# Optimization experiments

Measured on AMD Instinct MI355X. Metric: run time of the kernel, lower is better.

The kernel has to match this reference:

```python
import jax, jax.numpy as jnp
import numpy as np

B, N, D, H, P = 8, 1025, 768, 12, 32  # n = P*P + 1 (CLS + patches)
HD = D // H
EPS = 1e-5


def setup_inputs() -> dict:
    key = jax.random.key(0)
    ks = jax.random.split(key, 6)
    return {
        "x": jax.random.normal(ks[0], (B, N, D), dtype=jnp.float32),
        "canny": jax.random.uniform(ks[1], (B, 1, P, P), dtype=jnp.float32),
        "noise": jax.random.uniform(ks[2], (B, P, P), dtype=jnp.float32),
        "ln_w": jnp.ones((D,), dtype=jnp.float32),
        "ln_b": jnp.zeros((D,), dtype=jnp.float32),
        "w_qkv": (jax.random.normal(ks[3], (D, 3 * D), dtype=jnp.float32) * 0.02),
        "w_out": (jax.random.normal(ks[4], (D, D), dtype=jnp.float32) * 0.02),
        "b_out": jnp.zeros((D,), dtype=jnp.float32),
    }


def reference(x, canny, noise, ln_w, ln_b, w_qkv, w_out, b_out):
    b, n, d = x.shape
    # LayerNorm
    mu = jnp.mean(x, axis=-1, keepdims=True)
    var = jnp.mean(jnp.square(x - mu), axis=-1, keepdims=True)
    x_norm = (x - mu) * jax.lax.rsqrt(var + EPS) * ln_w + ln_b
    # QKV projection (no bias), split into heads: [b, n, 3, h, hd]
    qkv = (x_norm @ w_qkv).reshape(b, n, 3, H, HD)
    q = jnp.transpose(qkv[:, :, 0], (0, 2, 1, 3))  # [b, h, n, hd]
    k = jnp.transpose(qkv[:, :, 1], (0, 2, 1, 3))
    v = jnp.transpose(qkv[:, :, 2], (0, 2, 1, 3))
    # NOTE: source uses scale = dim ** -0.5 (full dim, not head_dim)
    dots = jnp.einsum('bhid,bhjd->bhij', q, k) * (d ** -0.5)
    # CLS-row prior injection: softmax over patch keys of CLS query row
    attn_row = jax.nn.softmax(dots[:, :, 0, 1:], axis=-1)  # [b, h, n-1]
    canny_flat = canny.reshape(b, -1) + 1.0                # [b, n-1]
    canny_flat = canny_flat / jnp.sum(canny_flat, axis=-1, keepdims=True)
    noise_flat = noise.reshape(b, -1)                      # [b, n-1]
    noise_flat = noise_flat / jnp.sum(noise_flat, axis=-1, keepdims=True)
    attn_row = attn_row + canny_flat[:, None, :] + noise_flat[:, None, :]
    dots = dots.at[:, :, 0, 1:].set(attn_row)
    # Second (full) softmax; dropout is identity in eval mode
    attn = jax.nn.softmax(dots, axis=-1)
    out = jnp.einsum('bhij,bhjd->bhid', attn, v)           # [b, h, n, hd]
    out = jnp.transpose(out, (0, 2, 1, 3)).reshape(b, n, d)
    return out @ w_out + b_out
```

## Files before the change

### kernel.cpp

```cpp
#include <hip/hip_runtime.h>

#define B_ 8
#define N_ 1025
#define D_ 768
#define H_ 12
#define NP_ 1024
#define ROWS_ (B_*N_)
#define ROWS_PAD_ 8320
#define QKVC_ 2304
#define SCALE_ 0.03608439182435161f
#define EPS_ 1e-5f

typedef float f32x4 __attribute__((ext_vector_type(4)));
typedef short s16x8 __attribute__((ext_vector_type(8)));

#define GLD16(g, l) __builtin_amdgcn_global_load_lds( \
    (const __attribute__((address_space(1))) unsigned int*)(g), \
    (__attribute__((address_space(3))) unsigned int*)(l), 16, 0, 0)

__device__ __forceinline__ float blo(unsigned int u){
  union { unsigned int i; float f; } v; v.i = u << 16; return v.f;
}
__device__ __forceinline__ float bhi(unsigned int u){
  union { unsigned int i; float f; } v; v.i = u & 0xffff0000u; return v.f;
}
__device__ __forceinline__ float bf2f(unsigned short u){
  union { unsigned int i; float f; } v; v.i = ((unsigned int)u) << 16; return v.f;
}
__device__ __forceinline__ unsigned short f2bf(float f){
  union { unsigned int i; float f; } v; v.f = f;
  unsigned int b = v.i;
  b = b + 0x7fffu + ((b >> 16) & 1u);
  return (unsigned short)(b >> 16);
}
__device__ __forceinline__ unsigned int pkbf2(float a, float b){
  union { float f; unsigned int i; } ua, ub;
  ua.f = a; ub.f = b;
  return __builtin_amdgcn_perm(ub.i + 0x8000u, ua.i + 0x8000u, 0x07060302u);
}

__global__ __launch_bounds__(256) void prep_fused(
    const float* __restrict__ w1, unsigned short* __restrict__ d1,
    const float* __restrict__ w2, unsigned short* __restrict__ d2,
    const float* __restrict__ x, const float* __restrict__ lw,
    const float* __restrict__ lb, unsigned short* __restrict__ xn) {
  int id = blockIdx.x;
  int t = threadIdx.x;
  if (id < 2304) {
    __shared__ unsigned short tile[32][33];
    int bx = id % 96;
    int kb = (id / 96) * 32;
    const float* src; unsigned short* dst; int N, nb;
    if (bx < 72) { src = w1; dst = d1; N = QKVC_; nb = bx * 32; }
    else         { src = w2; dst = d2; N = D_;    nb = (bx - 72) * 32; }
    int tx = t & 31, ty = t >> 5;
    #pragma unroll
    for (int i = 0; i < 4; i++) {
      int r = ty + i * 8;
      tile[r][tx] = f2bf(src[(size_t)(kb + r) * N + nb + tx]);
    }
    __syncthreads();
    #pragma unroll
    for (int i = 0; i < 4; i++) {
      int r = ty + i * 8;
      dst[(size_t)(nb + r) * D_ + kb + tx] = tile[tx][r];
    }
  } else {
    int row = id - 2304;
    __shared__ float r6[6];
    float4 v; float s = 0.f, q = 0.f;
    if (t < 192) {
      v = ((const float4*)(x + (size_t)row * D_))[t];
      s = v.x + v.y + v.z + v.w;
      q = v.x * v.x + v.y * v.y + v.z * v.z + v.w * v.w;
      #pragma unroll
      for (int off = 32; off > 0; off >>= 1) {
        s += __shfl_xor(s, off, 64);
        q += __shfl_xor(q, off, 64);
      }
      if ((t & 63) == 0) { r6[t >> 6] = s; r6[3 + (t >> 6)] = q; }
    }
    __syncthreads();
    if (t < 192) {
      s = r6[0] + r6[1] + r6[2];
      q = r6[3] + r6[4] + r6[5];
      float mean = s * (1.0f / 768.0f);
      float var = q * (1.0f / 768.0f) - mean * mean;
      var = var < 0.f ? 0.f : var;
      float rstd = rsqrtf(var + EPS_);
      float4 wv4 = ((const float4*)lw)[t];
      float4 bv4 = ((const float4*)lb)[t];
      float o0 = (v.x - mean) * rstd * wv4.x + bv4.x;
      float o1 = (v.y - mean) * rstd * wv4.y + bv4.y;
      float o2 = (v.z - mean) * rstd * wv4.z + bv4.z;
      float o3 = (v.w - mean) * rstd * wv4.w + bv4.w;
      uint2 pk = {pkbf2(o0, o1), pkbf2(o2, o3)};
      *(uint2*)(xn + (size_t)row * D_ + t * 4) = pk;
    }
  }
}

template <bool OF32>
__global__ __launch_bounds__(512) void gemm_bt(
    const unsigned short* __restrict__ A, const unsigned short* __restrict__ Bt,
    void* __restrict__ Cv, const float* __restrict__ bias,
    int Mvalid, int Nn, int Kk) {
  __shared__ short sh[32768];
  int t = threadIdx.x;
  int lane = t & 63, w = t >> 6;
  int m16 = lane & 15, quad = lane >> 4;

  int nwg = gridDim.x;
  int nbx = Nn >> 7;
  int id = blockIdx.x;
  int qq = nwg >> 3, rr = nwg & 7;
  int xcd = id & 7, off = id >> 3;
  int wg = (xcd < rr ? xcd * (qq + 1) : rr * (qq + 1) + (xcd - rr) * qq) + off;
  int bx = wg % nbx, by = wg / nbx;
  int bm = by * 128, bn = bx * 128;

  int wm = (w & 1) * 64, wn = (w >> 1) * 32;

  f32x4 acc[4][2];
  #pragma unroll
  for (int i = 0; i < 4; i++)
    #pragma unroll
    for (int j = 0; j < 2; j++) acc[i][j] = (f32x4){0.f, 0.f, 0.f, 0.f};

  const unsigned short* aP[2];
  const unsigned short* bP[2];
  #pragma unroll
  for (int c = 0; c < 2; c++) {
    int g = t + c * 512;
    int row = g >> 3, slot = g & 7;
    aP[c] = A  + (size_t)(bm + row) * Kk + ((slot ^ (row & 7)) * 8);
    bP[c] = Bt + (size_t)(bn + row) * Kk + ((slot ^ (row & 7)) * 8);
  }

  int KS = Kk >> 6;
  int cur = 0;
  #pragma unroll
  for (int c = 0; c < 2; c++) GLD16(aP[c], sh + (t + c * 512) * 8);
  #pragma unroll
  for (int c = 0; c < 2; c++) GLD16(bP[c], sh + 16384 + (t + c * 512) * 8);

  for (int kt = 0; kt < KS; kt++) {
    asm volatile("s_waitcnt vmcnt(0)" ::: "memory");
    __builtin_amdgcn_s_barrier();
    if (kt + 1 < KS) {
      int nb2 = (cur ^ 1) * 8192;
      int ko = (kt + 1) * 64;
      #pragma unroll
      for (int c = 0; c < 2; c++) GLD16(aP[c] + ko, sh + nb2 + (t + c * 512) * 8);
      #pragma unroll
      for (int c = 0; c < 2; c++) GLD16(bP[c] + ko, sh + 16384 + nb2 + (t + c * 512) * 8);
    }
    const short* sa = sh + cur * 8192;
    const short* sb = sh + 16384 + cur * 8192;
    #pragma unroll
    for (int ks = 0; ks < 2; ks++) {
      int so = ((ks * 4 + quad) ^ (m16 & 7)) * 8;
      s16x8 af[4], bfr[2];
      #pragma unroll
      for (int i = 0; i < 4; i++)
        af[i] = *(const s16x8*)(sa + (wm + i * 16 + m16) * 64 + so);
      #pragma unroll
      for (int j = 0; j < 2; j++)
        bfr[j] = *(const s16x8*)(sb + (wn + j * 16 + m16) * 64 + so);
      __builtin_amdgcn_s_setprio(1);
      #pragma unroll
      for (int i = 0; i < 4; i++)
        #pragma unroll
        for (int j = 0; j < 2; j++)
          acc[i][j] = __builtin_amdgcn_mfma_f32_16x16x32_bf16(af[i], bfr[j], acc[i][j], 0, 0, 0);
      __builtin_amdgcn_s_setprio(0);
    }
    cur ^= 1;
  }
  __syncthreads();

  if (!OF32) {
    unsigned short* C = (unsigned short*)Cv;
    #pragma unroll
    for (int j = 0; j < 2; j++) {
      int col = wn + j * 16 + m16;
      #pragma unroll
      for (int i = 0; i < 4; i++)
        #pragma unroll
        for (int r = 0; r < 4; r++)
          sh[(wm + i * 16 + quad * 4 + r) * 128 + col] = (short)f2bf(acc[i][j][r]);
    }
    __syncthreads();
    #pragma unroll
    for (int c = 0; c < 4; c++) {
      int idx = c * 512 + t;
      int row = idx >> 4, col = (idx & 15) * 8;
      if (bm + row < Mvalid)
        *(uint4*)(&C[(size_t)(bm + row) * Nn + bn + col]) = *(const uint4*)(&sh[row * 128 + col]);
    }
  } else {
    float* Cf = (float*)Cv;
    float* shf = (float*)sh;
    #pragma unroll
    for (int j = 0; j < 2; j++) {
      int col = wn + j * 16 + m16;
      float bv = bias ? bias[bn + col] : 0.f;
      #pragma unroll
      for (int i = 0; i < 4; i++)
        #pragma unroll
        for (int r = 0; r < 4; r++)
          shf[(wm + i * 16 + quad * 4 + r) * 128 + col] = acc[i][j][r] + bv;
    }
    __syncthreads();
    #pragma unroll
    for (int c = 0; c < 8; c++) {
      int idx = c * 512 + t;
      int row = idx >> 5, col = (idx & 31) * 4;
      if (bm + row < Mvalid)
        *(float4*)(&Cf[(size_t)(bm + row) * Nn + bn + col]) =
            *(const float4*)(&shf[row * 128 + col]);
    }
  }
}

__device__ __forceinline__ float block_sum(float v, float* red) {
  int t = threadIdx.x;
  red[t] = v;
  __syncthreads();
  for (int st = 128; st > 0; st >>= 1) {
    if (t < st) red[t] += red[t + st];
    __syncthreads();
  }
  float r = red[0];
  __syncthreads();
  return r;
}

__global__ __launch_bounds__(256) void attn_fused(
    const unsigned short* __restrict__ qkv, const float* __restrict__ canny,
    const float* __restrict__ noise, unsigned short* __restrict__ attn_out) {
  __shared__ __align__(16) char pool[37888];
  int id = blockIdx.x;
  int t = threadIdx.x;

  if (id < 768) {
    short* ps = (short*)pool;
    short* ks = (short*)(pool + 18432);
    unsigned int* vs = (unsigned int*)(pool + 27648);
    float* tailbuf = (float*)(pool + 36864);

    int tile = id / 96;
    int rem = id % 96;
    int h = rem >> 3;
    int b = rem & 7;
    int lane = t & 63, w = t >> 6;
    int m16 = lane & 15, quad = lane >> 4;

    int qbase = 1 + tile * 128;

    {
      int r = t >> 1, seg = (t & 1) * 32;
      const uint4* src = (const uint4*)(qkv + (size_t)(b * N_ + qbase + r) * QKVC_ + h * 64 + seg);
      uint4 u0 = src[0], u1 = src[1], u2 = src[2], u3 = src[3];
      *(uint4*)(&ps[r * 72 + seg])      = u0;
      *(uint4*)(&ps[r * 72 + seg + 8])  = u1;
      *(uint4*)(&ps[r * 72 + seg + 16]) = u2;
      *(uint4*)(&ps[r * 72 + seg + 24]) = u3;
    }
    s16x8 qb[2][2];
    #pragma unroll
    for (int nt = 0; nt < 2; nt++)
      #pragma unroll
      for (int ks_ = 0; ks_ < 2; ks_++) {
        qb[nt][ks_] = *(const s16x8*)(&ps[(w * 32 + nt * 16 + m16) * 72 + ks_ * 32 + quad * 8]);
        unsigned int* u = (unsigned int*)&qb[nt][ks_];
        #pragma unroll
        for (int i = 0; i < 4; i++)
          u[i] = pkbf2(blo(u[i]) * SCALE_, bhi(u[i]) * SCALE_);
      }
    s16x8 vone;
    #pragma unroll
    for (int i = 0; i < 8; i++) vone[i] = (short)0x3F80;

    f32x4 oacc[2][4], lacc[2];
    #pragma unroll
    for (int mt = 0; mt < 2; mt++) {
      lacc[mt] = (f32x4){0.f, 0.f, 0.f, 0.f};
      #pragma unroll
      for (int dt = 0; dt < 4; dt++) oacc[mt][dt] = (f32x4){0.f, 0.f, 0.f, 0.f};
    }

    int kkey = t >> 2, kseg = (t & 3) * 16;
    const unsigned short* kbase = qkv + (size_t)(b * N_) * QKVC_ + D_ + h * 64;
    int vp2 = t & 31, vseg = t >> 5;
    const unsigned short* vbase = qkv + (size_t)(b * N_) * QKVC_ + 2 * D_ + h * 64 + vseg * 8;
    uint4 kr0, kr1, vr0, vr1;
    {
      const uint4* ksrc = (const uint4*)(kbase + (size_t)kkey * QKVC_ + kseg);
      kr0 = ksrc[0]; kr1 = ksrc[1];
      vr0 = *(const uint4*)(vbase + (size_t)(2 * vp2) * QKVC_);
      vr1 = *(const uint4*)(vbase + (size_t)(2 * vp2 + 1) * QKVC_);
    }

    for (int jt = 0; jt < 16; jt++) {
      __syncthreads();
      *(uint4*)(&ks[kkey * 72 + kseg])     = kr0;
      *(uint4*)(&ks[kkey * 72 + kseg + 8]) = kr1;
      {
        const unsigned int* vaw = (const unsigned int*)&vr0;
        const unsigned int* vbw = (const unsigned int*)&vr1;
        #pragma unroll
        for (int i = 0; i < 4; i++) {
          vs[(vseg * 8 + 2 * i)     * 36 + vp2] = __builtin_amdgcn_perm(vbw[i], vaw[i], 0x05040100u);
          vs[(vseg * 8 + 2 * i + 1) * 36 + vp2] = __builtin_amdgcn_perm(vbw[i], vaw[i], 0x07060302u);
        }
      }
      __syncthreads();
      if (jt < 15) {
        int j0 = (jt + 1) * 64;
        const uint4* ksrc = (const uint4*)(kbase + (size_t)(j0 + kkey) * QKVC_ + kseg);
        kr0 = ksrc[0]; kr1 = ksrc[1];
        vr0 = *(const uint4*)(vbase + (size_t)(j0 + 2 * vp2) * QKVC_);
        vr1 = *(const uint4*)(vbase + (size_t)(j0 + 2 * vp2 + 1) * QKVC_);
      }
      f32x4 sacc[4][2];
      #pragma unroll
      for (int kt = 0; kt < 4; kt++) {
        s16x8 ka0 = *(const s16x8*)(&ks[(kt * 16 + m16) * 72 + quad * 8]);
        s16x8 ka1 = *(const s16x8*)(&ks[(kt * 16 + m16) * 72 + 32 + quad * 8]);
        #pragma unroll
        for (int nt = 0; nt < 2; nt++) {
          f32x4 s = (f32x4){0.f, 0.f, 0.f, 0.f};
          s = __builtin_amdgcn_mfma_f32_16x16x32_bf16(ka0, qb[nt][0], s, 0, 0, 0);
          s = __builtin_amdgcn_mfma_f32_16x16x32_bf16(ka1, qb[nt][1], s, 0, 0, 0);
          sacc[kt][nt] = s;
        }
      }
      #pragma unroll
      for (int kt = 0; kt < 4; kt++) {
        #pragma unroll
        for (int nt = 0; nt < 2; nt++) {
          f32x4 s = sacc[kt][nt];
          float p0 = __expf(s[0]);
          float p1 = __expf(s[1]);
          float p2 = __expf(s[2]);
          float p3 = __expf(s[3]);
          uint2 pk = {pkbf2(p0, p1), pkbf2(p2, p3)};
          *(uint2*)(&ps[(w * 32 + nt * 16 + m16) * 72 + kt * 16 + quad * 4]) = pk;
        }
      }
      __syncthreads();
      s16x8 pa[2][2];
      #pragma unroll
      for (int mt = 0; mt < 2; mt++)
        #pragma unroll
        for (int ks_ = 0; ks_ < 2; ks_++)
          pa[mt][ks_] = *(const s16x8*)(&ps[(w * 32 + mt * 16 + m16) * 72 + ks_ * 32 + quad * 8]);
      const short* vss = (const short*)vs;
      #pragma unroll
      for (int dt = 0; dt < 4; dt++) {
        s16x8 vb0 = *(const s16x8*)(&vss[(dt * 16 + m16) * 72 + quad * 8]);
        s16x8 vb1 = *(const s16x8*)(&vss[(dt * 16 + m16) * 72 + 32 + quad * 8]);
        #pragma unroll
        for (int mt = 0; mt < 2; mt++) {
          oacc[mt][dt] = __builtin_amdgcn_mfma_f32_16x16x32_bf16(pa[mt][0], vb0, oacc[mt][dt], 0, 0, 0);
          oacc[mt][dt] = __builtin_amdgcn_mfma_f32_16x16x32_bf16(pa[mt][1], vb1, oacc[mt][dt], 0, 0, 0);
        }
      }
      #pragma unroll
      for (int mt = 0; mt < 2; mt++) {
        lacc[mt] = __builtin_amdgcn_mfma_f32_16x16x32_bf16(pa[mt][0], vone, lacc[mt], 0, 0, 0);
        lacc[mt] = __builtin_amdgcn_mfma_f32_16x16x32_bf16(pa[mt][1], vone, lacc[mt], 0, 0, 0);
      }
    }
    if (t < 64)       tailbuf[t]             = bf2f(qkv[(size_t)(b * N_ + 1024) * QKVC_ + D_     + h * 64 + t]);
    else if (t < 128) tailbuf[64 + (t - 64)] = bf2f(qkv[(size_t)(b * N_ + 1024) * QKVC_ + 2 * D_ + h * 64 + (t - 64)]);
    __syncthreads();
    #pragma unroll
    for (int nt = 0; nt < 2; nt++) {
      float d = 0.f;
      #pragma unroll
      for (int jj = 0; jj < 8; jj++) {
        d += bf2f((unsigned short)qb[nt][0][jj]) * tailbuf[quad * 8 + jj];
        d += bf2f((unsigned short)qb[nt][1][jj]) * tailbuf[32 + quad * 8 + jj];
      }
      d += __shfl_xor(d, 16, 64);
      d += __shfl_xor(d, 32, 64);
      float p = __expf(d);
      if (quad == 0) tailbuf[128 + w * 32 + nt * 16 + m16] = p;
    }
    __syncthreads();
    #pragma unroll
    for (int mt = 0; mt < 2; mt++)
      #pragma unroll
      for (int r = 0; r < 4; r++) {
        float pr = tailbuf[128 + w * 32 + mt * 16 + quad * 4 + r];
        lacc[mt][r] += pr;
        #pragma unroll
        for (int dt = 0; dt < 4; dt++)
          oacc[mt][dt][r] += pr * tailbuf[64 + dt * 16 + m16];
      }
    #pragma unroll
    for (int mt = 0; mt < 2; mt++) {
      float rinv[4];
      #pragma unroll
      for (int r = 0; r < 4; r++) rinv[r] = 1.0f / lacc[mt][r];
      #pragma unroll
      for (int dt = 0; dt < 4; dt++) {
        #pragma unroll
        for (int r = 0; r < 4; r++) {
          int grow = b * N_ + qbase + w * 32 + mt * 16 + quad * 4 + r;
          attn_out[(size_t)grow * D_ + h * 64 + dt * 16 + m16] = f2bf(oacc[mt][dt][r] * rinv[r]);
        }
      }
    }
  } else {
    float* s     = (float*)pool;
    float* red   = (float*)(pool + 4608);
    float* q     = (float*)(pool + 5632);
    float* pvred = (float*)(pool + 5888);

    int bh = id - 768;
    int b = bh / H_, h = bh % H_;

    if (t < 64) q[t] = bf2f(qkv[(size_t)(b * N_) * QKVC_ + h * 64 + t]);
    __syncthreads();

    for (int j = t; j < N_; j += 256) {
      const unsigned short* krow = qkv + (size_t)(b * N_ + j) * QKVC_ + D_ + h * 64;
      float dot = 0.f;
      #pragma unroll
      for (int c = 0; c < 8; c++) {
        uint4 kk = *(const uint4*)(krow + c * 8);
        dot += q[c*8+0]*blo(kk.x) + q[c*8+1]*bhi(kk.x)
             + q[c*8+2]*blo(kk.y) + q[c*8+3]*bhi(kk.y)
             + q[c*8+4]*blo(kk.z) + q[c*8+5]*bhi(kk.z)
             + q[c*8+6]*blo(kk.w) + q[c*8+7]*bhi(kk.w);
      }
      s[j] = dot * SCALE_;
    }
    float cp = 0.f, npp = 0.f;
    for (int j = t; j < NP_; j += 256) {
      cp  += canny[b * NP_ + j] + 1.0f;
      npp += noise[b * NP_ + j];
    }
    float csum = block_sum(cp, red);
    float nsum = block_sum(npp, red);
    float e1 = 0.f;
    for (int j = t; j < N_; j += 256) if (j >= 1) e1 += __expf(s[j]);
    float sum1 = block_sum(e1, red);
    for (int j = t; j < N_; j += 256) {
      if (j >= 1) {
        s[j] = __expf(s[j]) / sum1
             + (canny[b * NP_ + j - 1] + 1.0f) / csum
             + noise[b * NP_ + j - 1] / nsum;
      }
    }
    __syncthreads();
    float e2 = 0.f;
    for (int j = t; j < N_; j += 256) { float e = __expf(s[j]); s[j] = e; e2 += e; }
    float sum2 = block_sum(e2, red);
    {
      int o = t & 7, g = t >> 3;
      float a[8] = {0.f, 0.f, 0.f, 0.f, 0.f, 0.f, 0.f, 0.f};
      for (int j = g; j < N_; j += 32) {
        float sv = s[j];
        uint4 vv = *(const uint4*)(qkv + (size_t)(b * N_ + j) * QKVC_ + 2 * D_ + h * 64 + o * 8);
        a[0] += sv * blo(vv.x); a[1] += sv * bhi(vv.x);
        a[2] += sv * blo(vv.y); a[3] += sv * bhi(vv.y);
        a[4] += sv * blo(vv.z); a[5] += sv * bhi(vv.z);
        a[6] += sv * blo(vv.w); a[7] += sv * bhi(vv.w);
      }
      #pragma unroll
      for (int i = 0; i < 8; i++) pvred[(o * 8 + i) * 33 + g] = a[i];
    }
    __syncthreads();
    if (t < 64) {
      float acc = 0.f;
      #pragma unroll
      for (int u = 0; u < 32; u++) acc += pvred[t * 33 + u];
      attn_out[(size_t)(b * N_) * D_ + h * 64 + t] = f2bf(acc / sum2);
    }
  }
}

extern "C" void kernel_launch(void* const* d_in, const int* in_sizes, int n_in,
                              void* d_out, int out_size, void* d_ws, size_t ws_size,
                              hipStream_t stream) {
  (void)in_sizes; (void)n_in; (void)out_size; (void)ws_size;
  const float* x     = (const float*)d_in[0];
  const float* canny = (const float*)d_in[1];
  const float* noise = (const float*)d_in[2];
  const float* lnw   = (const float*)d_in[3];
  const float* lnb   = (const float*)d_in[4];
  const float* wqkv  = (const float*)d_in[5];
  const float* wout  = (const float*)d_in[6];
  const float* bout  = (const float*)d_in[7];
  float* out = (float*)d_out;
  char* ws = (char*)d_ws;

  unsigned short* xn    = (unsigned short*)(ws);
  unsigned short* wqkvT = (unsigned short*)(ws + 12779520);
  unsigned short* woutT = (unsigned short*)(ws + 16318464);
  unsigned short* qkv   = (unsigned short*)(ws + 17498112);

  prep_fused<<<dim3(2304 + ROWS_), 256, 0, stream>>>(
      wqkv, wqkvT, wout, woutT, x, lnw, lnb, xn);
  gemm_bt<false><<<dim3((QKVC_ / 128) * (ROWS_PAD_ / 128)), 512, 0, stream>>>(
      xn, wqkvT, (void*)qkv, nullptr, ROWS_, QKVC_, D_);
  attn_fused<<<dim3(768 + B_ * H_), 256, 0, stream>>>(qkv, canny, noise, xn);
  gemm_bt<true><<<dim3((D_ / 128) * (ROWS_PAD_ / 128)), 512, 0, stream>>>(
      xn, woutT, (void*)out, bout, ROWS_, D_, D_);
}
```

Measured before the change: 198.2 us.

## Use 512-thread attention blocks with one 16-row query tile per wave

Doubles the attention kernel's block size from 256 to 512 threads, so each of 8 waves handles 16 query rows instead of 32. K/V tile loads, the CLS-row path and the reductions are re-partitioned across the extra threads, and the reduction scratch offsets grow to match. The aim is more waves in flight to hide latency and fewer registers per wave. In exchange each wave has less MFMA work per K/V tile, and syncs now span a larger block.

After: 210.8 us. 6.4% more time.

```diff
diff --git a/kernel.cpp b/kernel.cpp
--- a/kernel.cpp
+++ b/kernel.cpp
@@ -223,11 +223,11 @@
   }
 }
 
-__device__ __forceinline__ float block_sum(float v, float* red) {
+__device__ __forceinline__ float block_sum512(float v, float* red) {
   int t = threadIdx.x;
   red[t] = v;
   __syncthreads();
-  for (int st = 128; st > 0; st >>= 1) {
+  for (int st = 256; st > 0; st >>= 1) {
     if (t < st) red[t] += red[t + st];
     __syncthreads();
   }
@@ -236,7 +236,7 @@
   return r;
 }
 
-__global__ __launch_bounds__(256) void attn_fused(
+__global__ __launch_bounds__(512) void attn_fused(
     const unsigned short* __restrict__ qkv, const float* __restrict__ canny,
     const float* __restrict__ noise, unsigned short* __restrict__ attn_out) {
   __shared__ __align__(16) char pool[37888];
@@ -259,166 +259,138 @@
     int qbase = 1 + tile * 128;
 
     {
-      int r = t >> 1, seg = (t & 1) * 32;
+      int r = t >> 2, seg = (t & 3) * 16;
       const uint4* src = (const uint4*)(qkv + (size_t)(b * N_ + qbase + r) * QKVC_ + h * 64 + seg);
-      uint4 u0 = src[0], u1 = src[1], u2 = src[2], u3 = src[3];
-      *(uint4*)(&ps[r * 72 + seg])      = u0;
-      *(uint4*)(&ps[r * 72 + seg + 8])  = u1;
-      *(uint4*)(&ps[r * 72 + seg + 16]) = u2;
-      *(uint4*)(&ps[r * 72 + seg + 24]) = u3;
-    }
-    s16x8 qb[2][2];
-    #pragma unroll
-    for (int nt = 0; nt < 2; nt++)
-      #pragma unroll
-      for (int ks_ = 0; ks_ < 2; ks_++) {
-        qb[nt][ks_] = *(const s16x8*)(&ps[(w * 32 + nt * 16 + m16) * 72 + ks_ * 32 + quad * 8]);
-        unsigned int* u = (unsigned int*)&qb[nt][ks_];
-        #pragma unroll
-        for (int i = 0; i < 4; i++)
-          u[i] = pkbf2(blo(u[i]) * SCALE_, bhi(u[i]) * SCALE_);
-      }
+      uint4 u0 = src[0], u1 = src[1];
+      *(uint4*)(&ps[r * 72 + seg])     = u0;
+      *(uint4*)(&ps[r * 72 + seg + 8]) = u1;
+    }
+    s16x8 qb[2];
+    #pragma unroll
+    for (int ks_ = 0; ks_ < 2; ks_++) {
+      qb[ks_] = *(const s16x8*)(&ps[(w * 16 + m16) * 72 + ks_ * 32 + quad * 8]);
+      unsigned int* u = (unsigned int*)&qb[ks_];
+      #pragma unroll
+      for (int i = 0; i < 4; i++)
+        u[i] = pkbf2(blo(u[i]) * SCALE_, bhi(u[i]) * SCALE_);
+    }
     s16x8 vone;
     #pragma unroll
     for (int i = 0; i < 8; i++) vone[i] = (short)0x3F80;
 
-    f32x4 oacc[2][4], lacc[2];
-    #pragma unroll
-    for (int mt = 0; mt < 2; mt++) {
-      lacc[mt] = (f32x4){0.f, 0.f, 0.f, 0.f};
-      #pragma unroll
-      for (int dt = 0; dt < 4; dt++) oacc[mt][dt] = (f32x4){0.f, 0.f, 0.f, 0.f};
-    }
-
-    int kkey = t >> 2, kseg = (t & 3) * 16;
+    f32x4 oacc[4], lacc;
+    lacc = (f32x4){0.f, 0.f, 0.f, 0.f};
+    #pragma unroll
+    for (int dt = 0; dt < 4; dt++) oacc[dt] = (f32x4){0.f, 0.f, 0.f, 0.f};
+
+    int kkey = t >> 3, kseg = (t & 7) * 8;
     const unsigned short* kbase = qkv + (size_t)(b * N_) * QKVC_ + D_ + h * 64;
     int vp2 = t & 31, vseg = t >> 5;
-    const unsigned short* vbase = qkv + (size_t)(b * N_) * QKVC_ + 2 * D_ + h * 64 + vseg * 8;
-    uint4 kr0, kr1, vr0, vr1;
+    const unsigned short* vbase = qkv + (size_t)(b * N_) * QKVC_ + 2 * D_ + h * 64 + vseg * 4;
+    uint4 kr0; uint2 vr0, vr1;
     {
-      const uint4* ksrc = (const uint4*)(kbase + (size_t)kkey * QKVC_ + kseg);
-      kr0 = ksrc[0]; kr1 = ksrc[1];
-      vr0 = *(const uint4*)(vbase + (size_t)(2 * vp2) * QKVC_);
-      vr1 = *(const uint4*)(vbase + (size_t)(2 * vp2 + 1) * QKVC_);
+      kr0 = *(const uint4*)(kbase + (size_t)kkey * QKVC_ + kseg);
+      vr0 = *(const uint2*)(vbase + (size_t)(2 * vp2) * QKVC_);
+      vr1 = *(const uint2*)(vbase + (size_t)(2 * vp2 + 1) * QKVC_);
     }
 
     for (int jt = 0; jt < 16; jt++) {
       __syncthreads();
-      *(uint4*)(&ks[kkey * 72 + kseg])     = kr0;
-      *(uint4*)(&ks[kkey * 72 + kseg + 8]) = kr1;
+      *(uint4*)(&ks[kkey * 72 + kseg]) = kr0;
       {
         const unsigned int* vaw = (const unsigned int*)&vr0;
         const unsigned int* vbw = (const unsigned int*)&vr1;
         #pragma unroll
-        for (int i = 0; i < 4; i++) {
-          vs[(vseg * 8 + 2 * i)     * 36 + vp2] = __builtin_amdgcn_perm(vbw[i], vaw[i], 0x05040100u);
-          vs[(vseg * 8 + 2 * i + 1) * 36 + vp2] = __builtin_amdgcn_perm(vbw[i], vaw[i], 0x07060302u);
+        for (int i = 0; i < 2; i++) {
+          vs[(vseg * 4 + 2 * i)     * 36 + vp2] = __builtin_amdgcn_perm(vbw[i], vaw[i], 0x05040100u);
+          vs[(vseg * 4 + 2 * i + 1) * 36 + vp2] = __builtin_amdgcn_perm(vbw[i], vaw[i], 0x07060302u);
         }
       }
       __syncthreads();
       if (jt < 15) {
         int j0 = (jt + 1) * 64;
-        const uint4* ksrc = (const uint4*)(kbase + (size_t)(j0 + kkey) * QKVC_ + kseg);
-        kr0 = ksrc[0]; kr1 = ksrc[1];
-        vr0 = *(const uint4*)(vbase + (size_t)(j0 + 2 * vp2) * QKVC_);
-        vr1 = *(const uint4*)(vbase + (size_t)(j0 + 2 * vp2 + 1) * QKVC_);
-      }
-      f32x4 sacc[4][2];
+        kr0 = *(const uint4*)(kbase + (size_t)(j0 + kkey) * QKVC_ + kseg);
+        vr0 = *(const uint2*)(vbase + (size_t)(j0 + 2 * vp2) * QKVC_);
+        vr1 = *(const uint2*)(vbase + (size_t)(j0 + 2 * vp2 + 1) * QKVC_);
+      }
+      f32x4 sacc[4];
       #pragma unroll
       for (int kt = 0; kt < 4; kt++) {
         s16x8 ka0 = *(const s16x8*)(&ks[(kt * 16 + m16) * 72 + quad * 8]);
         s16x8 ka1 = *(const s16x8*)(&ks[(kt * 16 + m16) * 72 + 32 + quad * 8]);
-        #pragma unroll
-        for (int nt = 0; nt < 2; nt++) {
-          f32x4 s = (f32x4){0.f, 0.f, 0.f, 0.f};
-          s = __builtin_amdgcn_mfma_f32_16x16x32_bf16(ka0, qb[nt][0], s, 0, 0, 0);
-          s = __builtin_amdgcn_mfma_f32_16x16x32_bf16(ka1, qb[nt][1], s, 0, 0, 0);
-          sacc[kt][nt] = s;
-        }
+        f32x4 s = (f32x4){0.f, 0.f, 0.f, 0.f};
+        s = __builtin_amdgcn_mfma_f32_16x16x32_bf16(ka0, qb[0], s, 0, 0, 0);
+        s = __builtin_amdgcn_mfma_f32_16x16x32_bf16(ka1, qb[1], s, 0, 0, 0);
+        sacc[kt] = s;
       }
       #pragma unroll
       for (int kt = 0; kt < 4; kt++) {
-        #pragma unroll
-        for (int nt = 0; nt < 2; nt++) {
-          f32x4 s = sacc[kt][nt];
-          float p0 = __expf(s[0]);
-          float p1 = __expf(s[1]);
-          float p2 = __expf(s[2]);
-          float p3 = __expf(s[3]);
-          uint2 pk = {pkbf2(p0, p1), pkbf2(p2, p3)};
-          *(uint2*)(&ps[(w * 32 + nt * 16 + m16) * 72 + kt * 16 + quad * 4]) = pk;
-        }
+        f32x4 s = sacc[kt];
+        float p0 = __expf(s[0]);
+        float p1 = __expf(s[1]);
+        float p2 = __expf(s[2]);
+        float p3 = __expf(s[3]);
+        uint2 pk = {pkbf2(p0, p1), pkbf2(p2, p3)};
+        *(uint2*)(&ps[(w * 16 + m16) * 72 + kt * 16 + quad * 4]) = pk;
       }
       __syncthreads();
-      s16x8 pa[2][2];
-      #pragma unroll
-      for (int mt = 0; mt < 2; mt++)
-        #pragma unroll
-        for (int ks_ = 0; ks_ < 2; ks_++)
-          pa[mt][ks_] = *(const s16x8*)(&ps[(w * 32 + mt * 16 + m16) * 72 + ks_ * 32 + quad * 8]);
+      s16x8 pa[2];
+      #pragma unroll
+      for (int ks_ = 0; ks_ < 2; ks_++)
+        pa[ks_] = *(const s16x8*)(&ps[(w * 16 + m16) * 72 + ks_ * 32 + quad * 8]);
       const short* vss = (const short*)vs;
       #pragma unroll
       for (int dt = 0; dt < 4; dt++) {
         s16x8 vb0 = *(const s16x8*)(&vss[(dt * 16 + m16) * 72 + quad * 8]);
         s16x8 vb1 = *(const s16x8*)(&vss[(dt * 16 + m16) * 72 + 32 + quad * 8]);
-        #pragma unroll
-        for (int mt = 0; mt < 2; mt++) {
-          oacc[mt][dt] = __builtin_amdgcn_mfma_f32_16x16x32_bf16(pa[mt][0], vb0, oacc[mt][dt], 0, 0, 0);
-          oacc[mt][dt] = __builtin_amdgcn_mfma_f32_16x16x32_bf16(pa[mt][1], vb1, oacc[mt][dt], 0, 0, 0);
-        }
-      }
-      #pragma unroll
-      for (int mt = 0; mt < 2; mt++) {
-        lacc[mt] = __builtin_amdgcn_mfma_f32_16x16x32_bf16(pa[mt][0], vone, lacc[mt], 0, 0, 0);
-        lacc[mt] = __builtin_amdgcn_mfma_f32_16x16x32_bf16(pa[mt][1], vone, lacc[mt], 0, 0, 0);
-      }
+        oacc[dt] = __builtin_amdgcn_mfma_f32_16x16x32_bf16(pa[0], vb0, oacc[dt], 0, 0, 0);
+        oacc[dt] = __builtin_amdgcn_mfma_f32_16x16x32_bf16(pa[1], vb1, oacc[dt], 0, 0, 0);
+      }
+      lacc = __builtin_amdgcn_mfma_f32_16x16x32_bf16(pa[0], vone, lacc, 0, 0, 0);
+      lacc = __builtin_amdgcn_mfma_f32_16x16x32_bf16(pa[1], vone, lacc, 0, 0, 0);
     }
     if (t < 64)       tailbuf[t]             = bf2f(qkv[(size_t)(b * N_ + 1024) * QKVC_ + D_     + h * 64 + t]);
     else if (t < 128) tailbuf[64 + (t - 64)] = bf2f(qkv[(size_t)(b * N_ + 1024) * QKVC_ + 2 * D_ + h * 64 + (t - 64)]);
     __syncthreads();
-    #pragma unroll
-    for (int nt = 0; nt < 2; nt++) {
+    {
       float d = 0.f;
       #pragma unroll
       for (int jj = 0; jj < 8; jj++) {
-        d += bf2f((unsigned short)qb[nt][0][jj]) * tailbuf[quad * 8 + jj];
-        d += bf2f((unsigned short)qb[nt][1][jj]) * tailbuf[32 + quad * 8 + jj];
+        d += bf2f((unsigned short)qb[0][jj]) * tailbuf[quad * 8 + jj];
+        d += bf2f((unsigned short)qb[1][jj]) * tailbuf[32 + quad * 8 + jj];
       }
       d += __shfl_xor(d, 16, 64);
       d += __shfl_xor(d, 32, 64);
       float p = __expf(d);
-      if (quad == 0) tailbuf[128 + w * 32 + nt * 16 + m16] = p;
-    }
-    __syncthreads();
-    #pragma unroll
-    for (int mt = 0; mt < 2; mt++)
-      #pragma unroll
-      for (int r = 0; r < 4; r++) {
-        float pr = tailbuf[128 + w * 32 + mt * 16 + quad * 4 + r];
-        lacc[mt][r] += pr;
-        #pragma unroll
-        for (int dt = 0; dt < 4; dt++)
-          oacc[mt][dt][r] += pr * tailbuf[64 + dt * 16 + m16];
-      }
-    #pragma unroll
-    for (int mt = 0; mt < 2; mt++) {
+      if (quad == 0) tailbuf[128 + w * 16 + m16] = p;
+    }
+    __syncthreads();
+    #pragma unroll
+    for (int r = 0; r < 4; r++) {
+      float pr = tailbuf[128 + w * 16 + quad * 4 + r];
+      lacc[r] += pr;
+      #pragma unroll
+      for (int dt = 0; dt < 4; dt++)
+        oacc[dt][r] += pr * tailbuf[64 + dt * 16 + m16];
+    }
+    {
       float rinv[4];
       #pragma unroll
-      for (int r = 0; r < 4; r++) rinv[r] = 1.0f / lacc[mt][r];
+      for (int r = 0; r < 4; r++) rinv[r] = 1.0f / lacc[r];
       #pragma unroll
       for (int dt = 0; dt < 4; dt++) {
         #pragma unroll
         for (int r = 0; r < 4; r++) {
-          int grow = b * N_ + qbase + w * 32 + mt * 16 + quad * 4 + r;
-          attn_out[(size_t)grow * D_ + h * 64 + dt * 16 + m16] = f2bf(oacc[mt][dt][r] * rinv[r]);
+          int grow = b * N_ + qbase + w * 16 + quad * 4 + r;
+          attn_out[(size_t)grow * D_ + h * 64 + dt * 16 + m16] = f2bf(oacc[dt][r] * rinv[r]);
         }
       }
     }
   } else {
     float* s     = (float*)pool;
     float* red   = (float*)(pool + 4608);
-    float* q     = (float*)(pool + 5632);
-    float* pvred = (float*)(pool + 5888);
+    float* q     = (float*)(pool + 6656);
+    float* pvred = (float*)(pool + 6912);
 
     int bh = id - 768;
     int b = bh / H_, h = bh % H_;
@@ -426,7 +398,7 @@
     if (t < 64) q[t] = bf2f(qkv[(size_t)(b * N_) * QKVC_ + h * 64 + t]);
     __syncthreads();
 
-    for (int j = t; j < N_; j += 256) {
+    for (int j = t; j < N_; j += 512) {
       const unsigned short* krow = qkv + (size_t)(b * N_ + j) * QKVC_ + D_ + h * 64;
       float dot = 0.f;
       #pragma unroll
@@ -440,16 +412,16 @@
       s[j] = dot * SCALE_;
     }
     float cp = 0.f, npp = 0.f;
-    for (int j = t; j < NP_; j += 256) {
+    for (int j = t; j < NP_; j += 512) {
       cp  += canny[b * NP_ + j] + 1.0f;
       npp += noise[b * NP_ + j];
     }
-    float csum = block_sum(cp, red);
-    float nsum = block_sum(npp, red);
+    float csum = block_sum512(cp, red);
+    float nsum = block_sum512(npp, red);
     float e1 = 0.f;
-    for (int j = t; j < N_; j += 256) if (j >= 1) e1 += __expf(s[j]);
-    float sum1 = block_sum(e1, red);
-    for (int j = t; j < N_; j += 256) {
+    for (int j = t; j < N_; j += 512) if (j >= 1) e1 += __expf(s[j]);
+    float sum1 = block_sum512(e1, red);
+    for (int j = t; j < N_; j += 512) {
       if (j >= 1) {
         s[j] = __expf(s[j]) / sum1
              + (canny[b * NP_ + j - 1] + 1.0f) / csum
@@ -458,12 +430,12 @@
     }
     __syncthreads();
     float e2 = 0.f;
-    for (int j = t; j < N_; j += 256) { float e = __expf(s[j]); s[j] = e; e2 += e; }
-    float sum2 = block_sum(e2, red);
+    for (int j = t; j < N_; j += 512) { float e = __expf(s[j]); s[j] = e; e2 += e; }
+    float sum2 = block_sum512(e2, red);
     {
       int o = t & 7, g = t >> 3;
       float a[8] = {0.f, 0.f, 0.f, 0.f, 0.f, 0.f, 0.f, 0.f};
-      for (int j = g; j < N_; j += 32) {
+      for (int j = g; j < N_; j += 64) {
         float sv = s[j];
         uint4 vv = *(const uint4*)(qkv + (size_t)(b * N_ + j) * QKVC_ + 2 * D_ + h * 64 + o * 8);
         a[0] += sv * blo(vv.x); a[1] += sv * bhi(vv.x);
@@ -472,13 +444,13 @@
         a[6] += sv * blo(vv.w); a[7] += sv * bhi(vv.w);
       }
       #pragma unroll
-      for (int i = 0; i < 8; i++) pvred[(o * 8 + i) * 33 + g] = a[i];
+      for (int i = 0; i < 8; i++) pvred[(o * 8 + i) * 65 + g] = a[i];
     }
     __syncthreads();
     if (t < 64) {
       float acc = 0.f;
       #pragma unroll
-      for (int u = 0; u < 32; u++) acc += pvred[t * 33 + u];
+      for (int u = 0; u < 64; u++) acc += pvred[t * 65 + u];
       attn_out[(size_t)(b * N_) * D_ + h * 64 + t] = f2bf(acc / sum2);
     }
   }
@@ -508,7 +480,7 @@
       wqkv, wqkvT, wout, woutT, x, lnw, lnb, xn);
   gemm_bt<false><<<dim3((QKVC_ / 128) * (ROWS_PAD_ / 128)), 512, 0, stream>>>(
       xn, wqkvT, (void*)qkv, nullptr, ROWS_, QKVC_, D_);
-  attn_fused<<<dim3(768 + B_ * H_), 256, 0, stream>>>(qkv, canny, noise, xn);
+  attn_fused<<<dim3(768 + B_ * H_), 512, 0, stream>>>(qkv, canny, noise, xn);
   gemm_bt<true><<<dim3((D_ / 128) * (ROWS_PAD_ / 128)), 512, 0, stream>>>(
       xn, woutT, (void*)out, bout, ROWS_, D_, D_);
 }
```
